# Performance work log

Hardware: AMD Instinct MI355X
Metric: run time of the kernel (lower is better)

## Reference

```python
import jax, jax.numpy as jnp
import numpy as np

H = 16        # GRU hidden / attn embed dim
EPS = 1e-5    # BatchNorm eps


def setup_inputs() -> dict:
    key = jax.random.key(0)
    ks = jax.random.split(key, 24)
    B, T = 32768, 50
    s = 0.1
    inp = {
        "user_id": jax.random.randint(ks[0], (B,), 0, 10000),
        "history_item_id": jax.random.randint(ks[1], (B, T), 0, 10000),
        "history_category_id": jax.random.randint(ks[2], (B, T), 0, 10),
        "target_item_id": jax.random.randint(ks[3], (B, 1), 0, 10000),
        "target_category_id": jax.random.randint(ks[4], (B, 1), 0, 10),
        # embedding tables
        "user_table": jax.random.normal(ks[5], (10000, 16)) * s,
        "item_table": jax.random.normal(ks[6], (10000, 12)) * s,
        "cat_table": jax.random.normal(ks[7], (10, 4)) * s,
        # GRU (torch layout: [3H, in], gates order r,z,n)
        "gru_Wih": jax.random.normal(ks[8], (3 * H, H)) * s,
        "gru_Whh": jax.random.normal(ks[9], (3 * H, H)) * s,
        "gru_bih": jax.random.normal(ks[10], (3 * H,)) * s,
        "gru_bhh": jax.random.normal(ks[11], (3 * H,)) * s,
        # MultiheadAttention, 1 head, embed 16 (in_proj packs q,k,v)
        "mha_Win": jax.random.normal(ks[12], (3 * H, H)) * s,
        "mha_bin": jax.random.normal(ks[13], (3 * H,)) * s,
        "mha_Wout": jax.random.normal(ks[14], (H, H)) * s,
        "mha_bout": jax.random.normal(ks[15], (H,)) * s,
        # BN(48) -> Linear(48,16) -> ReLU -> BN(16) -> Linear(16,2) -> Softmax
        "bn1_g": jnp.ones((48,)),
        "bn1_b": jnp.zeros((48,)),
        "fc1_W": jax.random.normal(ks[16], (16, 48)) * s,
        "fc1_b": jax.random.normal(ks[17], (16,)) * s,
        "bn2_g": jnp.ones((16,)),
        "bn2_b": jnp.zeros((16,)),
        "fc2_W": jax.random.normal(ks[18], (2, 16)) * s,
        "fc2_b": jax.random.normal(ks[19], (2,)) * s,
    }
    return inp


def _gru(x, Wih, Whh, bih, bhh):
    # x: [B, T, H] -> outputs [B, T, H]; torch GRU cell math
    xg = jnp.einsum("bti,gi->btg", x, Wih) + bih           # [B,T,3H]
    xg = jnp.moveaxis(xg, 1, 0)                             # [T,B,3H]
    h0 = jnp.zeros((x.shape[0], H), x.dtype)

    def step(h, xt):
        hg = h @ Whh.T + bhh                                # [B,3H]
        xr, xz, xn = jnp.split(xt, 3, axis=-1)
        hr, hz, hn = jnp.split(hg, 3, axis=-1)
        r = jax.nn.sigmoid(xr + hr)
        z = jax.nn.sigmoid(xz + hz)
        n = jnp.tanh(xn + r * hn)
        h = (1.0 - z) * n + z * h
        return h, h

    _, ys = jax.lax.scan(step, h0, xg)
    return jnp.moveaxis(ys, 0, 1)                           # [B,T,H]


def _mha(q_in, kv_in, Win, bin_, Wout, bout):
    # single-head attention, batch_first
    Wq, Wk, Wv = jnp.split(Win, 3, axis=0)
    bq, bk, bv = jnp.split(bin_, 3, axis=0)
    q = q_in @ Wq.T + bq                                    # [B,T,H]
    k = kv_in @ Wk.T + bk                                   # [B,S,H]
    v = kv_in @ Wv.T + bv                                   # [B,S,H]
    scores = jnp.einsum("btd,bsd->bts", q, k) / jnp.sqrt(jnp.asarray(H, q.dtype))
    attn = jax.nn.softmax(scores, axis=-1)
    ctx = jnp.einsum("bts,bsd->btd", attn, v)
    return ctx @ Wout.T + bout                              # [B,T,H]


def _bn(x, g, b):
    # training-mode BatchNorm1d over batch axis
    mu = x.mean(axis=0)
    var = x.var(axis=0)
    return (x - mu) * jax.lax.rsqrt(var + EPS) * g + b


def reference(user_id, history_item_id, history_category_id, target_item_id,
              target_category_id, user_table, item_table, cat_table,
              gru_Wih, gru_Whh, gru_bih, gru_bhh,
              mha_Win, mha_bin, mha_Wout, mha_bout,
              bn1_g, bn1_b, fc1_W, fc1_b, bn2_g, bn2_b, fc2_W, fc2_b):
    user_emb = user_table[user_id]                          # [B,16]
    hist_emb = jnp.concatenate(
        [item_table[history_item_id], cat_table[history_category_id]], axis=-1)  # [B,T,16]
    tgt_emb = jnp.concatenate(
        [item_table[target_item_id], cat_table[target_category_id]], axis=-1)    # [B,1,16]

    hist_enc = _gru(hist_emb, gru_Wih, gru_Whh, gru_bih, gru_bhh)                 # [B,T,16]
    attn = _mha(hist_enc, tgt_emb, mha_Win, mha_bin, mha_Wout, mha_bout)          # [B,T,16]
    avg = (attn * hist_enc).sum(axis=1)                                           # [B,16]

    all_enc = jnp.concatenate([avg, tgt_emb[:, 0, :], user_emb], axis=1)          # [B,48]
    h = _bn(all_enc, bn1_g, bn1_b)
    h = jax.nn.relu(h @ fc1_W.T + fc1_b)
    h = _bn(h, bn2_g, bn2_b)
    logits = h @ fc2_W.T + fc2_b
    return jax.nn.softmax(logits, axis=-1)                                        # [B,2]
```

## Files before the change

kernel.cpp:

```cpp
#include <hip/hip_runtime.h>

#define BN_EPS 1e-5f

typedef const float* fp;
typedef float f32x4 __attribute__((ext_vector_type(4)));
typedef _Float16 f16x2 __attribute__((ext_vector_type(2)));
typedef _Float16 f16x4 __attribute__((ext_vector_type(4)));
typedef _Float16 f16x8 __attribute__((ext_vector_type(8)));

__device__ __forceinline__ float frcp(float x) { return __builtin_amdgcn_rcpf(x); }
__device__ __forceinline__ float sigm(float x) { return frcp(1.0f + __expf(-x)); }
__device__ __forceinline__ float tanh_fast(float x) { return 1.0f - 2.0f * frcp(1.0f + __expf(2.0f * x)); }

__device__ __forceinline__ f32x4 ld4(const float* p) { return *(const f32x4*)p; }
__device__ __forceinline__ float dot4(f32x4 a, f32x4 b) {
    return a[0] * b[0] + a[1] * b[1] + a[2] * b[2] + a[3] * b[3];
}

#define MFMA16(A, B, C) __builtin_amdgcn_mfma_f32_16x16x16f16((A), (B), (C), 0, 0, 0)
#define MFMA32(A, B, C) __builtin_amdgcn_mfma_f32_16x16x32_f16((A), (B), (C), 0, 0, 0)

#define GLDS16(gp, lp) __builtin_amdgcn_global_load_lds( \
    (const __attribute__((address_space(1))) void*)(gp), \
    (__attribute__((address_space(3))) void*)(lp), 16, 0, 0)

__device__ __forceinline__ f16x4 pk_f16(f32x4 v) {
    f16x2 lo = __builtin_bit_cast(f16x2, __builtin_amdgcn_cvt_pkrtz(v[0], v[1]));
    f16x2 hi = __builtin_bit_cast(f16x2, __builtin_amdgcn_cvt_pkrtz(v[2], v[3]));
    return __builtin_shufflevector(lo, hi, 0, 1, 2, 3);
}

__global__ __launch_bounds__(256) void k_precompute(
    fp Wih, fp bih, fp bhh, fp item_table, fp cat_table,
    float* __restrict__ itemP, float* __restrict__ P_cat,
    float* __restrict__ stats, int nPadElems, int nPadBlocks)
{
    if ((int)blockIdx.x < nPadBlocks) {
        int idx = blockIdx.x * blockDim.x + threadIdx.x;
        if (idx < nPadElems) {
            int i = idx >> 4, j = idx & 15;
            itemP[idx] = (j < 12) ? item_table[i * 12 + j] : 0.f;
        }
    } else {
        for (int t = threadIdx.x; t < 480; t += blockDim.x) {
            int c = t / 48, g = t % 48;
            float acc = bih[g] + (g < 32 ? bhh[g] : 0.f);
#pragma unroll
            for (int k = 0; k < 4; ++k) acc += Wih[g * 16 + 12 + k] * cat_table[c * 4 + k];
            P_cat[c * 52 + g] = acc;
        }
        if (threadIdx.x < 128) stats[threadIdx.x] = 0.f;
    }
}

__global__ __launch_bounds__(256, 2) void k_gru(
    const int* __restrict__ user_id, const int* __restrict__ hist_item,
    const int* __restrict__ hist_cat, const int* __restrict__ tgt_item,
    const int* __restrict__ tgt_cat,
    fp user_table, fp item_table, fp cat_table,
    fp Whh, fp bhh, fp Wih,
    fp mha_Win, fp mha_bin, fp mha_Wout, fp mha_bout,
    const float* __restrict__ itemP, const float* __restrict__ P_cat,
    float* __restrict__ all_enc, float* __restrict__ stats1, int B, int T)
{
    __shared__ float s_pcat[520];
    __shared__ float s_stage[4][4][256];
    __shared__ int   s_iid[4][1040];
    __shared__ int   s_cid[4][1040];
    __shared__ float lds_part[4][96];

    const int tid  = threadIdx.x;
    const int lane = tid & 63;
    const int wid  = tid >> 6;
    const int s    = lane & 15;
    const int hi   = lane >> 4;

    long b = (long)blockIdx.x * 64 + wid * 16 + s;
    const bool act = (b < B);
    if (!act) b = B - 1;

    for (int t = tid; t < 520; t += 256) s_pcat[t] = P_cat[t];

    const int ti  = tgt_item[b];
    const int tc  = tgt_cat[b];
    const int uid = user_id[b];

    {
        const int* ip = hist_item + b * T;
        const int* cp = hist_cat  + b * T;
        int* di = &s_iid[wid][s * 65];
        int* dc = &s_cid[wid][s * 65];
        for (int k = hi; k < T; k += 4) { di[k] = ip[k]; dc[k] = cp[k]; }
    }

    f32x4 whrf = ld4(&Whh[(0  + s) * 16 + 4 * hi]);
    f32x4 whzf = ld4(&Whh[(16 + s) * 16 + 4 * hi]);
    f32x4 whnf = ld4(&Whh[(32 + s) * 16 + 4 * hi]);
    f32x4 wirf = ld4(&Wih[(0  + s) * 16 + 4 * hi]);
    f32x4 wizf = ld4(&Wih[(16 + s) * 16 + 4 * hi]);
    f32x4 winf = ld4(&Wih[(32 + s) * 16 + 4 * hi]);
    f16x4 whr_h = __builtin_convertvector(whrf, f16x4);
    f16x4 whz_h = __builtin_convertvector(whzf, f16x4);
    f16x4 whn_h = __builtin_convertvector(whnf, f16x4);
    f16x4 wir_h = __builtin_convertvector(wirf, f16x4);
    f16x4 wiz_h = __builtin_convertvector(wizf, f16x4);
    f16x4 win_h = __builtin_convertvector(winf, f16x4);
    f16x4 whr_l = __builtin_convertvector(whrf - __builtin_convertvector(whr_h, f32x4), f16x4);
    f16x4 whz_l = __builtin_convertvector(whzf - __builtin_convertvector(whz_h, f32x4), f16x4);
    f16x4 whn_l = __builtin_convertvector(whnf - __builtin_convertvector(whn_h, f32x4), f16x4);
    f16x4 wir_l = __builtin_convertvector(wirf - __builtin_convertvector(wir_h, f32x4), f16x4);
    f16x4 wiz_l = __builtin_convertvector(wizf - __builtin_convertvector(wiz_h, f32x4), f16x4);
    f16x4 win_l = __builtin_convertvector(winf - __builtin_convertvector(win_h, f32x4), f16x4);
    f16x8 Ar  = __builtin_shufflevector(wir_h, whr_h, 0, 1, 2, 3, 4, 5, 6, 7);
    f16x8 ArL = __builtin_shufflevector(wir_l, whr_l, 0, 1, 2, 3, 4, 5, 6, 7);
    f16x8 Az  = __builtin_shufflevector(wiz_h, whz_h, 0, 1, 2, 3, 4, 5, 6, 7);
    f16x8 AzL = __builtin_shufflevector(wiz_l, whz_l, 0, 1, 2, 3, 4, 5, 6, 7);
    f16x8 Anx = __builtin_shufflevector(win_h, win_l, 0, 1, 2, 3, 4, 5, 6, 7);
    f16x8 Anh = __builtin_shufflevector(whn_h, whn_l, 0, 1, 2, 3, 4, 5, 6, 7);
    const f32x4 bhn4 = ld4(&bhh[32 + 4 * hi]);

    f32x4 h    = {0.f, 0.f, 0.f, 0.f};
    f32x4 hsum = {0.f, 0.f, 0.f, 0.f};
    f16x4 hh = {}, hl = {};

    __syncthreads();

    const int T1 = T - 1;
    const int so = s * 65;
    float* stg = &s_stage[wid][0][0];
    const int l4 = lane * 4;

#pragma unroll
    for (int d = 0; d < 4; ++d) {
        int td = (d > T1) ? T1 : d;
        int idd = s_iid[wid][so + td];
        GLDS16((const char*)itemP + (size_t)(unsigned)idd * 64u + hi * 16, stg + d * 256);
    }
    int cd = s_cid[wid][so];

    for (int t = 0; t < T; ++t) {
        int t4 = (t + 4 > T1) ? T1 : t + 4;
        int t1 = (t + 1 > T1) ? T1 : t + 1;
        int idn = s_iid[wid][so + t4];
        int cdn = s_cid[wid][so + t1];

        asm volatile("s_waitcnt vmcnt(3)" ::: "memory");

        float* bp = stg + (t & 3) * 256;
        f32x4 e4 = ld4(bp + l4);
        const float* pc = s_pcat + cd * 52 + 4 * hi;
        f32x4 pcr = ld4(pc), pcz = ld4(pc + 16), pcn = ld4(pc + 32);

        asm volatile("s_waitcnt lgkmcnt(0)" ::: "memory");

        GLDS16((const char*)itemP + (size_t)(unsigned)idn * 64u + hi * 16, bp);
        cd = cdn;

        f16x4 e_h = pk_f16(e4);
        f32x4 eb;
#pragma unroll
        for (int q = 0; q < 4; ++q) eb[q] = (float)e_h[q];
        f16x4 e_l = pk_f16(e4 - eb);

        f16x8 Bhh = __builtin_shufflevector(e_h, hh, 0, 1, 2, 3, 4, 5, 6, 7);
        f16x8 Bll = __builtin_shufflevector(e_l, hl, 0, 1, 2, 3, 4, 5, 6, 7);
        f16x8 Bee = __builtin_shufflevector(e_h, e_h, 0, 1, 2, 3, 0, 1, 2, 3);
        f16x8 Bh2 = __builtin_shufflevector(hh, hh, 0, 1, 2, 3, 0, 1, 2, 3);

        f32x4 aR = MFMA32(Ar, Bhh, MFMA32(Ar, Bll, MFMA32(ArL, Bhh, pcr)));
        f32x4 aZ = MFMA32(Az, Bhh, MFMA32(Az, Bll, MFMA32(AzL, Bhh, pcz)));
        f32x4 xn = MFMA16(win_h, e_l, MFMA32(Anx, Bee, pcn));
        f32x4 hn = MFMA16(whn_h, hl, MFMA32(Anh, Bh2, bhn4));

#pragma unroll
        for (int q = 0; q < 4; ++q) {
            float r = sigm(aR[q]);
            float z = sigm(aZ[q]);
            float n = tanh_fast(fmaf(r, hn[q], xn[q]));
            h[q] = z * (h[q] - n) + n;
        }
        hsum += h;
        hh = pk_f16(h);
        f32x4 hb;
#pragma unroll
        for (int q = 0; q < 4; ++q) hb[q] = (float)hh[q];
        hl = pk_f16(h - hb);
    }

    const float* itr = item_table + (size_t)ti * 12;
    f32x4 tv0 = ld4(itr), tv1 = ld4(itr + 4), tv2 = ld4(itr + 8);
    f32x4 tv3 = ld4(cat_table + tc * 4);

    f32x4 vq;
#pragma unroll
    for (int q = 0; q < 4; ++q) {
        int row = 32 + 4 * hi + q;
        const float* wv = mha_Win + row * 16;
        vq[q] = mha_bin[row] + dot4(ld4(wv), tv0) + dot4(ld4(wv + 4), tv1)
              + dot4(ld4(wv + 8), tv2) + dot4(ld4(wv + 12), tv3);
    }
    f32x4 vg0, vg1, vg2, vg3;
#pragma unroll
    for (int q = 0; q < 4; ++q) {
        vg0[q] = __shfl_xor(vq[q], (hi ^ 0) << 4);
        vg1[q] = __shfl_xor(vq[q], (hi ^ 1) << 4);
        vg2[q] = __shfl_xor(vq[q], (hi ^ 2) << 4);
        vg3[q] = __shfl_xor(vq[q], (hi ^ 3) << 4);
    }
    f32x4 aj;
#pragma unroll
    for (int q = 0; q < 4; ++q) {
        int row = 4 * hi + q;
        const float* wo = mha_Wout + row * 16;
        aj[q] = mha_bout[row] + dot4(ld4(wo), vg0) + dot4(ld4(wo + 4), vg1)
              + dot4(ld4(wo + 8), vg2) + dot4(ld4(wo + 12), vg3);
    }
    f32x4 avg = aj * hsum;

    f32x4 u4 = ld4(user_table + (size_t)uid * 16 + 4 * hi);
    f32x4 t4v = (hi == 0) ? tv0 : (hi == 1) ? tv1 : (hi == 2) ? tv2 : tv3;

    if (act) {
        float* er = all_enc + b * 48 + 4 * hi;
        *(f32x4*)er        = avg;
        *(f32x4*)(er + 16) = t4v;
        *(f32x4*)(er + 32) = u4;
    }

    const f32x4 zero4 = {0.f, 0.f, 0.f, 0.f};
    f32x4 sa = act ? avg : zero4, st = act ? t4v : zero4, su = act ? u4 : zero4;
    f32x4 qa = sa * sa, qt = st * st, qu = su * su;
#pragma unroll
    for (int m = 1; m <= 8; m <<= 1) {
#pragma unroll
        for (int q = 0; q < 4; ++q) {
            sa[q] += __shfl_xor(sa[q], m);
            st[q] += __shfl_xor(st[q], m);
            su[q] += __shfl_xor(su[q], m);
            qa[q] += __shfl_xor(qa[q], m);
            qt[q] += __shfl_xor(qt[q], m);
            qu[q] += __shfl_xor(qu[q], m);
        }
    }
    if (s == 0) {
        int c = 4 * hi;
#pragma unroll
        for (int q = 0; q < 4; ++q) {
            lds_part[wid][c + q]      = sa[q];
            lds_part[wid][16 + c + q] = st[q];
            lds_part[wid][32 + c + q] = su[q];
            lds_part[wid][48 + c + q] = qa[q];
            lds_part[wid][64 + c + q] = qt[q];
            lds_part[wid][80 + c + q] = qu[q];
        }
    }
    __syncthreads();
    if (tid < 96) {
        float v = lds_part[0][tid] + lds_part[1][tid] + lds_part[2][tid] + lds_part[3][tid];
        atomicAdd(&stats1[tid], v);
    }
}

__global__ __launch_bounds__(256) void k_fc1(
    const float* __restrict__ all_enc, const float* __restrict__ stats,
    fp fc1_W, fp fc1_b, fp g1, fp b1,
    float* __restrict__ hbuf, float* __restrict__ stats2, int B)
{
    const int tid = threadIdx.x, lane = tid & 63, wid = tid >> 6;
    const int j = lane & 15, sl = lane >> 4;
    __shared__ float kk[48], mm[48];
    __shared__ float part[4][32];

    if (tid < 48) {
        float mu  = stats[tid] / (float)B;
        float var = stats[48 + tid] / (float)B - mu * mu;
        float k   = rsqrtf(var + BN_EPS);
        float gk  = g1[tid] * k;
        kk[tid] = gk;
        mm[tid] = b1[tid] - mu * gk;
    }
    __syncthreads();

    float w[48];
    float bj = fc1_b[j];
#pragma unroll
    for (int q = 0; q < 12; ++q) {
        float4 v = *(const float4*)&fc1_W[j * 48 + q * 4];
        w[q * 4 + 0] = v.x * kk[q * 4 + 0];
        w[q * 4 + 1] = v.y * kk[q * 4 + 1];
        w[q * 4 + 2] = v.z * kk[q * 4 + 2];
        w[q * 4 + 3] = v.w * kk[q * 4 + 3];
        bj += v.x * mm[q * 4 + 0] + v.y * mm[q * 4 + 1]
            + v.z * mm[q * 4 + 2] + v.w * mm[q * 4 + 3];
    }

    float sh = 0.f, sq = 0.f;
    for (long b = (long)blockIdx.x * 16 + wid * 4 + sl; b < B; b += (long)gridDim.x * 16) {
        const float* x = all_enc + b * 48;
        float acc = bj;
#pragma unroll
        for (int q = 0; q < 12; ++q) {
            float4 v = *(const float4*)&x[q * 4];
            acc += w[q * 4] * v.x + w[q * 4 + 1] * v.y + w[q * 4 + 2] * v.z + w[q * 4 + 3] * v.w;
        }
        float h = fmaxf(acc, 0.f);
        hbuf[b * 16 + j] = h;
        sh += h; sq += h * h;
    }
    sh += __shfl_xor(sh, 16); sh += __shfl_xor(sh, 32);
    sq += __shfl_xor(sq, 16); sq += __shfl_xor(sq, 32);
    if (sl == 0) { part[wid][j] = sh; part[wid][16 + j] = sq; }
    __syncthreads();
    if (tid < 32) {
        float v = part[0][tid] + part[1][tid] + part[2][tid] + part[3][tid];
        atomicAdd(&stats2[tid], v);
    }
}

__global__ __launch_bounds__(256) void k_out(
    const float* __restrict__ hbuf, const float* __restrict__ stats2,
    fp fc2_W, fp fc2_b, fp g2, fp b2, float* __restrict__ out, int B)
{
    __shared__ float w[34];
    const int tid = threadIdx.x;
    if (tid < 32) {
        int c = tid & 15;
        float mu  = stats2[c] / (float)B;
        float var = stats2[16 + c] / (float)B - mu * mu;
        float gk  = g2[c] * rsqrtf(var + BN_EPS);
        w[tid] = fc2_W[tid] * gk;
    }
    if (tid < 2) {
        float acc = fc2_b[tid];
        for (int c = 0; c < 16; ++c) {
            float mu  = stats2[c] / (float)B;
            float var = stats2[16 + c] / (float)B - mu * mu;
            float gk  = g2[c] * rsqrtf(var + BN_EPS);
            acc += fc2_W[tid * 16 + c] * (b2[c] - mu * gk);
        }
        w[32 + tid] = acc;
    }
    __syncthreads();
    for (long b = (long)blockIdx.x * blockDim.x + threadIdx.x; b < B;
         b += (long)gridDim.x * blockDim.x) {
        const float* h = hbuf + b * 16;
        float l0 = w[32], l1 = w[33];
#pragma unroll
        for (int q = 0; q < 4; ++q) {
            float4 v = *(const float4*)&h[q * 4];
            l0 += w[q * 4] * v.x + w[q * 4 + 1] * v.y + w[q * 4 + 2] * v.z + w[q * 4 + 3] * v.w;
            l1 += w[16 + q * 4] * v.x + w[17 + q * 4] * v.y + w[18 + q * 4] * v.z + w[19 + q * 4] * v.w;
        }
        float m  = fmaxf(l0, l1);
        float e0 = __expf(l0 - m), e1 = __expf(l1 - m);
        float inv = frcp(e0 + e1);
        float2 p; p.x = e0 * inv; p.y = e1 * inv;
        *(float2*)&out[b * 2] = p;
    }
}

extern "C" void kernel_launch(void* const* d_in, const int* in_sizes, int n_in,
                              void* d_out, int out_size, void* d_ws, size_t ws_size,
                              hipStream_t stream)
{
    const int* user_id   = (const int*)d_in[0];
    const int* hist_item = (const int*)d_in[1];
    const int* hist_cat  = (const int*)d_in[2];
    const int* tgt_item  = (const int*)d_in[3];
    const int* tgt_cat   = (const int*)d_in[4];
    fp user_table = (fp)d_in[5];
    fp item_table = (fp)d_in[6];
    fp cat_table  = (fp)d_in[7];
    fp Wih = (fp)d_in[8],  Whh = (fp)d_in[9];
    fp bih = (fp)d_in[10], bhh = (fp)d_in[11];
    fp Win = (fp)d_in[12], binp = (fp)d_in[13];
    fp Wout = (fp)d_in[14], bout = (fp)d_in[15];
    fp g1 = (fp)d_in[16], b1 = (fp)d_in[17];
    fp fc1W = (fp)d_in[18], fc1b = (fp)d_in[19];
    fp g2 = (fp)d_in[20], b2 = (fp)d_in[21];
    fp fc2W = (fp)d_in[22], fc2b = (fp)d_in[23];

    const int B = in_sizes[0];
    const int T = in_sizes[1] / B;
    const int nItem = in_sizes[6] / 12;
    const int nPadElems = nItem * 16;

    float* ws      = (float*)d_ws;
    float* itemP   = ws;
    float* P_cat   = itemP + (size_t)nPadElems;
    float* stats   = P_cat + 520;
    float* stats2  = stats + 96;
    float* all_enc = stats + 128 + 8;
    float* hbuf    = all_enc + (size_t)B * 48;

    const int nPadBlocks = (nPadElems + 255) / 256;
    hipLaunchKernelGGL(k_precompute, dim3(nPadBlocks + 1), dim3(256), 0, stream,
                       Wih, bih, bhh, item_table, cat_table, itemP, P_cat, stats,
                       nPadElems, nPadBlocks);

    hipLaunchKernelGGL(k_gru, dim3((B + 63) / 64), dim3(256), 0, stream,
                       user_id, hist_item, hist_cat, tgt_item, tgt_cat,
                       user_table, item_table, cat_table, Whh, bhh, Wih,
                       Win, binp, Wout, bout, itemP, P_cat,
                       all_enc, stats, B, T);

    hipLaunchKernelGGL(k_fc1, dim3(512), dim3(256), 0, stream,
                       all_enc, stats, fc1W, fc1b, g1, b1, hbuf, stats2, B);

    hipLaunchKernelGGL(k_out, dim3((B + 255) / 256), dim3(256), 0, stream,
                       hbuf, stats2, fc2W, fc2b, g2, b2, (float*)d_out, B);
}
```

Measured before the change: 75.59 us.

## Gather item and category embeddings directly, drop padded-table precompute kernel

```diff
diff --git a/kernel.cpp b/kernel.cpp
--- a/kernel.cpp
+++ b/kernel.cpp
@@ -30,27 +30,52 @@
     return __builtin_shufflevector(lo, hi, 0, 1, 2, 3);
 }
 
-__global__ __launch_bounds__(256) void k_precompute(
-    fp Wih, fp bih, fp bhh, fp item_table, fp cat_table,
-    float* __restrict__ itemP, float* __restrict__ P_cat,
-    float* __restrict__ stats, int nPadElems, int nPadBlocks)
+__global__ void k_zero(float* __restrict__ stats) { stats[threadIdx.x] = 0.f; }
+
+__device__ __forceinline__ void gru_step_mf(
+    f32x4 e4,
+    const f16x8& Ar, const f16x8& ArL, const f16x8& Az, const f16x8& AzL,
+    const f16x8& Anx, const f16x8& Anh, const f16x4& winh, const f16x4& whnh,
+    const f32x4& br4, const f32x4& bz4, const f32x4& bxn4, const f32x4& bhn4,
+    f32x4& h, f32x4& hsum, f16x4& hh, f16x4& hl)
 {
-    if ((int)blockIdx.x < nPadBlocks) {
-        int idx = blockIdx.x * blockDim.x + threadIdx.x;
-        if (idx < nPadElems) {
-            int i = idx >> 4, j = idx & 15;
-            itemP[idx] = (j < 12) ? item_table[i * 12 + j] : 0.f;
-        }
-    } else {
-        for (int t = threadIdx.x; t < 480; t += blockDim.x) {
-            int c = t / 48, g = t % 48;
-            float acc = bih[g] + (g < 32 ? bhh[g] : 0.f);
-#pragma unroll
-            for (int k = 0; k < 4; ++k) acc += Wih[g * 16 + 12 + k] * cat_table[c * 4 + k];
-            P_cat[c * 52 + g] = acc;
-        }
-        if (threadIdx.x < 128) stats[threadIdx.x] = 0.f;
-    }
+    const f32x4 z4 = {0.f, 0.f, 0.f, 0.f};
+    f16x4 e_h = pk_f16(e4);
+    f32x4 eb;
+#pragma unroll
+    for (int q = 0; q < 4; ++q) eb[q] = (float)e_h[q];
+    f16x4 e_l = pk_f16(e4 - eb);
+    f16x8 Bhh = __builtin_shufflevector(e_h, hh, 0, 1, 2, 3, 4, 5, 6, 7);
+    f16x8 Bll = __builtin_shufflevector(e_l, hl, 0, 1, 2, 3, 4, 5, 6, 7);
+    f16x8 Bee = __builtin_shufflevector(e_h, e_h, 0, 1, 2, 3, 0, 1, 2, 3);
+    f16x8 Bh2 = __builtin_shufflevector(hh, hh, 0, 1, 2, 3, 0, 1, 2, 3);
+    f32x4 r0 = MFMA32(Ar,  Bhh, br4);
+    f32x4 r1 = MFMA32(ArL, Bhh, z4);
+    f32x4 r2 = MFMA32(Ar,  Bll, z4);
+    f32x4 zg0 = MFMA32(Az,  Bhh, bz4);
+    f32x4 zg1 = MFMA32(AzL, Bhh, z4);
+    f32x4 zg2 = MFMA32(Az,  Bll, z4);
+    f32x4 x0 = MFMA32(Anx, Bee, bxn4);
+    f32x4 x1 = MFMA16(winh, e_l, z4);
+    f32x4 n0 = MFMA32(Anh, Bh2, bhn4);
+    f32x4 n1 = MFMA16(whnh, hl, z4);
+    f32x4 aR = (r0 + r1) + r2;
+    f32x4 aZ = (zg0 + zg1) + zg2;
+    f32x4 xn = x0 + x1;
+    f32x4 hn = n0 + n1;
+#pragma unroll
+    for (int q = 0; q < 4; ++q) {
+        float r = sigm(aR[q]);
+        float z = sigm(aZ[q]);
+        float n = tanh_fast(fmaf(r, hn[q], xn[q]));
+        h[q] = z * (h[q] - n) + n;
+    }
+    hsum += h;
+    hh = pk_f16(h);
+    f32x4 hb;
+#pragma unroll
+    for (int q = 0; q < 4; ++q) hb[q] = (float)hh[q];
+    hl = pk_f16(h - hb);
 }
 
 __global__ __launch_bounds__(256, 2) void k_gru(
@@ -58,16 +83,13 @@
     const int* __restrict__ hist_cat, const int* __restrict__ tgt_item,
     const int* __restrict__ tgt_cat,
     fp user_table, fp item_table, fp cat_table,
-    fp Whh, fp bhh, fp Wih,
+    fp Whh, fp bhh, fp Wih, fp bih,
     fp mha_Win, fp mha_bin, fp mha_Wout, fp mha_bout,
-    const float* __restrict__ itemP, const float* __restrict__ P_cat,
     float* __restrict__ all_enc, float* __restrict__ stats1, int B, int T)
 {
-    __shared__ float s_pcat[520];
-    __shared__ float s_stage[4][4][256];
-    __shared__ int   s_iid[4][1040];
-    __shared__ int   s_cid[4][1040];
-    __shared__ float lds_part[4][96];
+    __shared__ float    s_stage[4][4][256];
+    __shared__ unsigned s_ids[4][16 * 67];
+    __shared__ float    lds_part[4][96];
 
     const int tid  = threadIdx.x;
     const int lane = tid & 63;
@@ -79,112 +101,89 @@
     const bool act = (b < B);
     if (!act) b = B - 1;
 
-    for (int t = tid; t < 520; t += 256) s_pcat[t] = P_cat[t];
-
     const int ti  = tgt_item[b];
     const int tc  = tgt_cat[b];
     const int uid = user_id[b];
+    asm volatile("" :: "v"(ti), "v"(tc), "v"(uid));
 
     {
         const int* ip = hist_item + b * T;
         const int* cp = hist_cat  + b * T;
-        int* di = &s_iid[wid][s * 65];
-        int* dc = &s_cid[wid][s * 65];
-        for (int k = hi; k < T; k += 4) { di[k] = ip[k]; dc[k] = cp[k]; }
-    }
-
+        unsigned* d = &s_ids[wid][s * 67];
+        for (int k = hi; k < T; k += 4)
+            d[k] = (unsigned)ip[k] | ((unsigned)cp[k] << 16);
+    }
+
+    f32x4 wirf = ld4(&Wih[(0  + s) * 16 + 4 * hi]);
+    f32x4 wizf = ld4(&Wih[(16 + s) * 16 + 4 * hi]);
+    f32x4 winf = ld4(&Wih[(32 + s) * 16 + 4 * hi]);
     f32x4 whrf = ld4(&Whh[(0  + s) * 16 + 4 * hi]);
     f32x4 whzf = ld4(&Whh[(16 + s) * 16 + 4 * hi]);
     f32x4 whnf = ld4(&Whh[(32 + s) * 16 + 4 * hi]);
-    f32x4 wirf = ld4(&Wih[(0  + s) * 16 + 4 * hi]);
-    f32x4 wizf = ld4(&Wih[(16 + s) * 16 + 4 * hi]);
-    f32x4 winf = ld4(&Wih[(32 + s) * 16 + 4 * hi]);
+    f16x4 wir_h = __builtin_convertvector(wirf, f16x4);
+    f16x4 wiz_h = __builtin_convertvector(wizf, f16x4);
+    f16x4 win_h = __builtin_convertvector(winf, f16x4);
     f16x4 whr_h = __builtin_convertvector(whrf, f16x4);
     f16x4 whz_h = __builtin_convertvector(whzf, f16x4);
     f16x4 whn_h = __builtin_convertvector(whnf, f16x4);
-    f16x4 wir_h = __builtin_convertvector(wirf, f16x4);
-    f16x4 wiz_h = __builtin_convertvector(wizf, f16x4);
-    f16x4 win_h = __builtin_convertvector(winf, f16x4);
+    f16x4 wir_l = __builtin_convertvector(wirf - __builtin_convertvector(wir_h, f32x4), f16x4);
+    f16x4 wiz_l = __builtin_convertvector(wizf - __builtin_convertvector(wiz_h, f32x4), f16x4);
+    f16x4 win_l = __builtin_convertvector(winf - __builtin_convertvector(win_h, f32x4), f16x4);
     f16x4 whr_l = __builtin_convertvector(whrf - __builtin_convertvector(whr_h, f32x4), f16x4);
     f16x4 whz_l = __builtin_convertvector(whzf - __builtin_convertvector(whz_h, f32x4), f16x4);
     f16x4 whn_l = __builtin_convertvector(whnf - __builtin_convertvector(whn_h, f32x4), f16x4);
-    f16x4 wir_l = __builtin_convertvector(wirf - __builtin_convertvector(wir_h, f32x4), f16x4);
-    f16x4 wiz_l = __builtin_convertvector(wizf - __builtin_convertvector(wiz_h, f32x4), f16x4);
-    f16x4 win_l = __builtin_convertvector(winf - __builtin_convertvector(win_h, f32x4), f16x4);
     f16x8 Ar  = __builtin_shufflevector(wir_h, whr_h, 0, 1, 2, 3, 4, 5, 6, 7);
     f16x8 ArL = __builtin_shufflevector(wir_l, whr_l, 0, 1, 2, 3, 4, 5, 6, 7);
     f16x8 Az  = __builtin_shufflevector(wiz_h, whz_h, 0, 1, 2, 3, 4, 5, 6, 7);
     f16x8 AzL = __builtin_shufflevector(wiz_l, whz_l, 0, 1, 2, 3, 4, 5, 6, 7);
     f16x8 Anx = __builtin_shufflevector(win_h, win_l, 0, 1, 2, 3, 4, 5, 6, 7);
     f16x8 Anh = __builtin_shufflevector(whn_h, whn_l, 0, 1, 2, 3, 4, 5, 6, 7);
+    const f32x4 br4  = ld4(&bih[4 * hi])      + ld4(&bhh[4 * hi]);
+    const f32x4 bz4  = ld4(&bih[16 + 4 * hi]) + ld4(&bhh[16 + 4 * hi]);
+    const f32x4 bxn4 = ld4(&bih[32 + 4 * hi]);
     const f32x4 bhn4 = ld4(&bhh[32 + 4 * hi]);
 
-    f32x4 h    = {0.f, 0.f, 0.f, 0.f};
-    f32x4 hsum = {0.f, 0.f, 0.f, 0.f};
+    f32x4 h = {0.f, 0.f, 0.f, 0.f}, hsum = {0.f, 0.f, 0.f, 0.f};
     f16x4 hh = {}, hl = {};
 
     __syncthreads();
 
     const int T1 = T - 1;
-    const int so = s * 65;
+    const unsigned* idsrow = &s_ids[wid][s * 67];
     float* stg = &s_stage[wid][0][0];
     const int l4 = lane * 4;
 
-#pragma unroll
-    for (int d = 0; d < 4; ++d) {
-        int td = (d > T1) ? T1 : d;
-        int idd = s_iid[wid][so + td];
-        GLDS16((const char*)itemP + (size_t)(unsigned)idd * 64u + hi * 16, stg + d * 256);
-    }
-    int cd = s_cid[wid][so];
+#define GADDR(pk) ((hi < 3) \
+    ? (const char*)item_table + (size_t)((pk) & 0xffffu) * 48u + hi * 16 \
+    : (const char*)cat_table  + (size_t)((pk) >> 16) * 16u)
+
+    {
+        unsigned p0 = idsrow[0];
+        unsigned p1 = idsrow[(1 > T1) ? T1 : 1];
+        unsigned p2 = idsrow[(2 > T1) ? T1 : 2];
+        unsigned p3 = idsrow[(3 > T1) ? T1 : 3];
+        GLDS16(GADDR(p0), stg);
+        GLDS16(GADDR(p1), stg + 256);
+        GLDS16(GADDR(p2), stg + 512);
+        GLDS16(GADDR(p3), stg + 768);
+    }
+    unsigned idcdA = idsrow[(4 > T1) ? T1 : 4];
+    asm volatile("s_waitcnt vmcnt(2)" ::: "memory");
+    f32x4 eCur = ld4(stg + l4);
 
     for (int t = 0; t < T; ++t) {
-        int t4 = (t + 4 > T1) ? T1 : t + 4;
-        int t1 = (t + 1 > T1) ? T1 : t + 1;
-        int idn = s_iid[wid][so + t4];
-        int cdn = s_cid[wid][so + t1];
-
-        asm volatile("s_waitcnt vmcnt(3)" ::: "memory");
-
-        float* bp = stg + (t & 3) * 256;
-        f32x4 e4 = ld4(bp + l4);
-        const float* pc = s_pcat + cd * 52 + 4 * hi;
-        f32x4 pcr = ld4(pc), pcz = ld4(pc + 16), pcn = ld4(pc + 32);
+        asm volatile("s_waitcnt vmcnt(2)" ::: "memory");
+        f32x4 eNext = ld4(stg + (((t + 1) & 3) << 8) + l4);
+        int t5 = (t + 5 > T1) ? T1 : t + 5;
+        unsigned idcdB = idsrow[t5];
+
+        gru_step_mf(eCur, Ar, ArL, Az, AzL, Anx, Anh, win_h, whn_h,
+                    br4, bz4, bxn4, bhn4, h, hsum, hh, hl);
 
         asm volatile("s_waitcnt lgkmcnt(0)" ::: "memory");
-
-        GLDS16((const char*)itemP + (size_t)(unsigned)idn * 64u + hi * 16, bp);
-        cd = cdn;
-
-        f16x4 e_h = pk_f16(e4);
-        f32x4 eb;
-#pragma unroll
-        for (int q = 0; q < 4; ++q) eb[q] = (float)e_h[q];
-        f16x4 e_l = pk_f16(e4 - eb);
-
-        f16x8 Bhh = __builtin_shufflevector(e_h, hh, 0, 1, 2, 3, 4, 5, 6, 7);
-        f16x8 Bll = __builtin_shufflevector(e_l, hl, 0, 1, 2, 3, 4, 5, 6, 7);
-        f16x8 Bee = __builtin_shufflevector(e_h, e_h, 0, 1, 2, 3, 0, 1, 2, 3);
-        f16x8 Bh2 = __builtin_shufflevector(hh, hh, 0, 1, 2, 3, 0, 1, 2, 3);
-
-        f32x4 aR = MFMA32(Ar, Bhh, MFMA32(Ar, Bll, MFMA32(ArL, Bhh, pcr)));
-        f32x4 aZ = MFMA32(Az, Bhh, MFMA32(Az, Bll, MFMA32(AzL, Bhh, pcz)));
-        f32x4 xn = MFMA16(win_h, e_l, MFMA32(Anx, Bee, pcn));
-        f32x4 hn = MFMA16(whn_h, hl, MFMA32(Anh, Bh2, bhn4));
-
-#pragma unroll
-        for (int q = 0; q < 4; ++q) {
-            float r = sigm(aR[q]);
-            float z = sigm(aZ[q]);
-            float n = tanh_fast(fmaf(r, hn[q], xn[q]));
-            h[q] = z * (h[q] - n) + n;
-        }
-        hsum += h;
-        hh = pk_f16(h);
-        f32x4 hb;
-#pragma unroll
-        for (int q = 0; q < 4; ++q) hb[q] = (float)hh[q];
-        hl = pk_f16(h - hb);
+        GLDS16(GADDR(idcdA), stg + ((t & 3) << 8));
+        idcdA = idcdB;
+        eCur  = eNext;
     }
 
     const float* itr = item_table + (size_t)ti * 12;
@@ -217,7 +216,7 @@
     }
     f32x4 avg = aj * hsum;
 
-    f32x4 u4 = ld4(user_table + (size_t)uid * 16 + 4 * hi);
+    f32x4 u4  = ld4(user_table + (size_t)uid * 16 + 4 * hi);
     f32x4 t4v = (hi == 0) ? tv0 : (hi == 1) ? tv1 : (hi == 2) ? tv2 : tv3;
 
     if (act) {
@@ -382,27 +381,19 @@
 
     const int B = in_sizes[0];
     const int T = in_sizes[1] / B;
-    const int nItem = in_sizes[6] / 12;
-    const int nPadElems = nItem * 16;
 
     float* ws      = (float*)d_ws;
-    float* itemP   = ws;
-    float* P_cat   = itemP + (size_t)nPadElems;
-    float* stats   = P_cat + 520;
+    float* stats   = ws;
     float* stats2  = stats + 96;
-    float* all_enc = stats + 128 + 8;
+    float* all_enc = stats + 128;
     float* hbuf    = all_enc + (size_t)B * 48;
 
-    const int nPadBlocks = (nPadElems + 255) / 256;
-    hipLaunchKernelGGL(k_precompute, dim3(nPadBlocks + 1), dim3(256), 0, stream,
-                       Wih, bih, bhh, item_table, cat_table, itemP, P_cat, stats,
-                       nPadElems, nPadBlocks);
+    hipLaunchKernelGGL(k_zero, dim3(1), dim3(128), 0, stream, stats);
 
     hipLaunchKernelGGL(k_gru, dim3((B + 63) / 64), dim3(256), 0, stream,
                        user_id, hist_item, hist_cat, tgt_item, tgt_cat,
-                       user_table, item_table, cat_table, Whh, bhh, Wih,
-                       Win, binp, Wout, bout, itemP, P_cat,
-                       all_enc, stats, B, T);
+                       user_table, item_table, cat_table, Whh, bhh, Wih, bih,
+                       Win, binp, Wout, bout, all_enc, stats, B, T);
 
     hipLaunchKernelGGL(k_fc1, dim3(512), dim3(256), 0, stream,
                        all_enc, stats, fc1W, fc1b, g1, b1, hbuf, stats2, B);
```

After: 74.85 us. Within noise of the previous version (-1.0%).
